# Kernel optimization log

Measured on AMD Instinct MI355X. Metric: run time of the kernel, lower is better.

Reference implementation:

```python
import jax, jax.numpy as jnp
import numpy as np
from jax import lax

H = 32      # n_heads
D = 128     # head_dim
HID = 4096  # hidden_dim
CQ, CK, CH = 4, 9, 2
G = H // CH  # conv groups == groupnorm groups == 16


def setup_inputs() -> dict:
    key = jax.random.key(0)
    ks = jax.random.split(key, 8)
    q_seqlen = np.array([512, 384, 384, 256], dtype=np.int64)
    kv_seqlen = np.array([512, 384, 384, 256], dtype=np.int64)
    Sq = int(q_seqlen.sum())
    Sk = int(kv_seqlen.sum())
    x = jax.random.normal(ks[0], (Sq, HID), dtype=jnp.float32) * 0.02
    context = jax.random.normal(ks[1], (Sk, HID), dtype=jnp.float32) * 0.02
    wq = jax.random.normal(ks[2], (HID, H * D), dtype=jnp.float32) * 0.02
    wkv = jax.random.normal(ks[3], (HID, 2 * H * D), dtype=jnp.float32) * 0.02
    wo = jax.random.normal(ks[4], (H * D, HID), dtype=jnp.float32) * 0.02
    # grouped conv kernel [out=H, in_per_group=CH, CQ, CK]; dirac-like identity + noise
    conv_w = jax.random.normal(ks[5], (H, CH, CQ, CK), dtype=jnp.float32) * 0.05
    conv_w = conv_w.at[jnp.arange(H), jnp.arange(H) % CH, CQ // 2, CK // 2].add(1.0)
    gn_w = jnp.ones((H,), dtype=jnp.float32)
    gn_b = jnp.zeros((H,), dtype=jnp.float32)
    return {"x": x, "context": context, "wq": wq, "wkv": wkv, "wo": wo,
            "conv_w": conv_w, "gn_w": gn_w, "gn_b": gn_b,
            "q_seqlen": q_seqlen, "kv_seqlen": kv_seqlen}


def _block_diag_mask(q_seqlen, kv_seqlen, dtype):
    # block-diagonal ones mask for packed ragged sequences (static lengths)
    q_len = np.asarray(q_seqlen)
    k_len = np.asarray(kv_seqlen)
    seg_q = np.repeat(np.arange(len(q_len)), q_len)
    seg_k = np.repeat(np.arange(len(k_len)), k_len)
    return jnp.asarray(seg_q[:, None] == seg_k[None, :], dtype=dtype)


def reference(x, context, wq, wkv, wo, conv_w, gn_w, gn_b, q_seqlen, kv_seqlen):
    S = x.shape[0]
    mask = _block_diag_mask(q_seqlen, kv_seqlen, x.dtype)  # [Sq, Sk]
    scale = 1.0 / np.sqrt(D).astype(np.float32)
    q = (x @ wq).reshape(S, H, D).transpose(1, 0, 2) * scale        # [H, Sq, D]
    kv = context @ wkv
    k = kv[:, : H * D].reshape(-1, H, D).transpose(1, 0, 2)         # [H, Sk, D]
    v = kv[:, H * D :].reshape(-1, H, D).transpose(1, 0, 2)         # [H, Sk, D]
    attn = jnp.einsum('hqd,hkd->hqk', q, k) * mask[None]            # [H, Sq, Sk]
    # grouped Conv2d over (query, key) positions, channels = heads
    a = lax.conv_general_dilated(
        attn[None], conv_w, window_strides=(1, 1),
        padding=((CQ // 2, CQ // 2), (CK // 2, CK // 2)),
        dimension_numbers=('NCHW', 'OIHW', 'NCHW'),
        feature_group_count=G)[0]                                   # [H, Sq+1, Sk]
    a = a[:, :-1, :]  # c_q even -> drop extra row (c_k odd -> no col drop)
    a = jax.nn.softmax(a + mask[None], axis=-1)                     # note: +1 bias inside blocks, not -inf
    out = jnp.einsum('hqk,hkd->hqd', a, v)                          # [H, Sq, D]
    # GroupNorm(num_groups=G, channels=H) over [1, H, Sq, D]
    og = out.reshape(G, CH, S, D)
    mu = og.mean(axis=(1, 2, 3), keepdims=True)
    var = og.var(axis=(1, 2, 3), keepdims=True)
    og = (og - mu) * lax.rsqrt(var + 1e-5)
    out = og.reshape(H, S, D) * gn_w[:, None, None] + gn_b[:, None, None]
    out = out.transpose(1, 0, 2).reshape(S, H * D)
    return out @ wo
```

## Files before the change

### kernel.cpp

```cpp
#include <hip/hip_runtime.h>
#include <stdint.h>


#define H_   32
#define D_   128
#define HID_ 4096
#define WMAX2 944
#define LPAD 8

typedef unsigned short bfr;
typedef __attribute__((ext_vector_type(4))) float f32x4;
typedef __attribute__((ext_vector_type(4))) int   i32x4;
typedef __attribute__((ext_vector_type(8))) unsigned short u16x8;
typedef __attribute__((ext_vector_type(4))) unsigned short u16x4;

__device__ __forceinline__ bfr f2bf(float f) {
  uint32_t u = __float_as_uint(f);
  u += 0x7fffu + ((u >> 16) & 1u);
  return (bfr)(u >> 16);
}
__device__ __forceinline__ float bf2f(bfr u) {
  return __uint_as_float(((uint32_t)u) << 16);
}
__device__ __forceinline__ void mfma_bf16(f32x4& d, i32x4 a, i32x4 b) {
  asm volatile("v_mfma_f32_16x16x32_bf16 %0, %1, %2, %0" : "+v"(d) : "v"(a), "v"(b));
}
__device__ __forceinline__ void gload_lds16(const void* g, void* l) {
  __builtin_amdgcn_global_load_lds((__attribute__((address_space(1))) void*)g,
                                   (__attribute__((address_space(3))) void*)l,
                                   16, 0, 0);
}

__global__ __launch_bounds__(256) void seg_setup(
    const void* __restrict__ qsl, const void* __restrict__ ksl,
    int* __restrict__ segq, int* __restrict__ segk,
    int* __restrict__ bq, int* __restrict__ bk,
    float* __restrict__ stats, int S, int Sk, int nseg)
{
  __shared__ int sbq[16], sbk[16];
  const int tid = threadIdx.x;
  if (tid == 0) {
    {
      const int* q32 = (const int*)qsl;
      long long s32 = 0; bool ok32 = true;
      for (int i = 0; i < nseg; ++i) { int v = q32[i]; if (v < 1 || v > S) ok32 = false; s32 += v; }
      const bool use32 = ok32 && (s32 == S);
      const long long* q64 = (const long long*)qsl;
      sbq[0] = 0;
      for (int i = 0; i < nseg; ++i) sbq[i + 1] = sbq[i] + (use32 ? q32[i] : (int)q64[i]);
    }
    {
      const int* k32 = (const int*)ksl;
      long long s32 = 0; bool ok32 = true;
      for (int i = 0; i < nseg; ++i) { int v = k32[i]; if (v < 1 || v > Sk) ok32 = false; s32 += v; }
      const bool use32 = ok32 && (s32 == Sk);
      const long long* k64 = (const long long*)ksl;
      sbk[0] = 0;
      for (int i = 0; i < nseg; ++i) sbk[i + 1] = sbk[i] + (use32 ? k32[i] : (int)k64[i]);
    }
    for (int i = 0; i <= nseg; ++i) { bq[i] = sbq[i]; bk[i] = sbk[i]; }
  }
  if (tid < 32) stats[tid] = 0.f;
  __syncthreads();
  for (int i = tid; i < S; i += 256) {
    int s = 0;
    while (s < nseg - 1 && i >= sbq[s + 1]) ++s;
    segq[i] = s;
  }
  for (int i = tid; i < Sk; i += 256) {
    int s = 0;
    while (s < nseg - 1 && i >= sbk[s + 1]) ++s;
    segk[i] = s;
  }
}

__global__ __launch_bounds__(256) void cvt_bf16(
    const float* __restrict__ in, bfr* __restrict__ out, long long n)
{
  long long i = ((long long)blockIdx.x * 256 + threadIdx.x) * 8;
  if (i >= n) return;
  f32x4 a = *(const f32x4*)(in + i);
  f32x4 b = *(const f32x4*)(in + i + 4);
  u16x8 o;
  #pragma unroll
  for (int j = 0; j < 4; ++j) { o[j] = f2bf(a[j]); o[4 + j] = f2bf(b[j]); }
  *(u16x8*)(out + i) = o;
}

__global__ __launch_bounds__(256) void transpose_cvt(
    const float* __restrict__ in, bfr* __restrict__ out, int R, int ld)
{
  __shared__ float tile[64][65];
  const int t = threadIdx.x;
  const int rb = blockIdx.y * 64, cb = blockIdx.x * 64;
  const int row = t >> 2, c4 = (t & 3) * 16;
  const float* gp = in + (long long)(rb + row) * ld + cb + c4;
  #pragma unroll
  for (int j = 0; j < 4; ++j) {
    f32x4 v = *(const f32x4*)(gp + j * 4);
    #pragma unroll
    for (int q = 0; q < 4; ++q) tile[row][c4 + j * 4 + q] = v[q];
  }
  __syncthreads();
  const int cc = row, r4 = c4;
  u16x8 a, b;
  #pragma unroll
  for (int j = 0; j < 8; ++j) a[j] = f2bf(tile[r4 + j][cc]);
  #pragma unroll
  for (int j = 0; j < 8; ++j) b[j] = f2bf(tile[r4 + 8 + j][cc]);
  bfr* op = out + (long long)(cb + cc) * R + rb + r4;
  *(u16x8*)op = a;
  *(u16x8*)(op + 8) = b;
}

__global__ __launch_bounds__(256) void transpose_b16(
    const bfr* __restrict__ in, bfr* __restrict__ out, int R, int C)
{
  __shared__ bfr t[64][72];
  const int z = blockIdx.z;
  const bfr* ip = in + (long long)z * R * C;
  bfr* op = out + (long long)z * R * C;
  const int rb = blockIdx.y * 64, cb = blockIdx.x * 64;
  const int tr = threadIdx.x >> 3;
  const int tc = (threadIdx.x & 7) * 8;
  #pragma unroll
  for (int half = 0; half < 2; ++half) {
    const int r = tr + half * 32;
    u16x8 v = *(const u16x8*)(ip + (long long)(rb + r) * C + cb + tc);
    *(u16x8*)&t[r][tc] = v;
  }
  __syncthreads();
  #pragma unroll
  for (int half = 0; half < 2; ++half) {
    const int cc = tr + half * 32;
    u16x8 vv;
    #pragma unroll
    for (int j = 0; j < 8; ++j) vv[j] = t[tc + j][cc];
    *(u16x8*)(op + (long long)(cb + cc) * R + rb + tc) = vv;
  }
}

__global__ __launch_bounds__(256) void colsum_v(
    const bfr* __restrict__ vt, float* __restrict__ cs, int Sk)
{
  const int lane = threadIdx.x & 63, wave = threadIdx.x >> 6;
  const int row = blockIdx.x * 4 + wave;
  const bfr* src = vt + (long long)row * Sk;
  float s = 0.f;
  for (int i = lane * 8; i + 8 <= Sk; i += 512) {
    u16x8 v = *(const u16x8*)(src + i);
    #pragma unroll
    for (int j = 0; j < 8; ++j) s += bf2f(v[j]);
  }
  #pragma unroll
  for (int m = 1; m < 64; m <<= 1) s += __shfl_xor(s, m);
  if (lane == 0) cs[row] = s;
}

struct GemmAux {
  const int* segq; const int* segk; const int* bk;
  bfr* qb; bfr* kb; bfr* vrow;
  float* outb; float* stats;
  const float* fvArr; const float* colsum;
  float scale;
  int S, Sk, nOff;
};

enum { MODE_PLAIN = 0, MODE_Q = 1, MODE_KV = 2, MODE_QK = 3, MODE_PV = 4 };

template <int MODE, int KS = 1>
__global__ __launch_bounds__(256) void gemm_bt(
    const bfr* __restrict__ A, const bfr* __restrict__ Bt, void* __restrict__ Cout,
    int N, int K, int lda, int ldb,
    long long aZ, long long bZ, long long cZ, GemmAux aux)
{
  __shared__ bfr As[128 * 32];
  __shared__ bfr Bs[128 * 32];
  __shared__ float redS[8], redSS[8];
  const int tid = threadIdx.x;
  const int lane = tid & 63;
  const int wave = tid >> 6;
  const int z = blockIdx.z;

  int bx = blockIdx.x, by = blockIdx.y;
  {
    const int gx = gridDim.x, gy = gridDim.y;
    if (((gx & 3) == 0) && ((gy & 1) == 0)) {
      const int lid = by * gx + bx;
      const int xcd = lid & 7, inner = lid >> 3;
      const int cm = gy >> 1, cn = gx >> 2;
      by = (xcd >> 2) * cm + inner / cn;
      bx = (xcd & 3) * cn + inner % cn;
    }
  }
  const int m0 = by * 128;
  const int n0 = bx * 128;
  const bfr* Ap = A + (long long)z * aZ;
  const bfr* Bp = Bt + (long long)z * bZ;

  int kLo = 0, kHiV = K;
  if constexpr (KS > 1) { const int ksp = K / KS; kLo = z * ksp; kHiV = kLo + ksp; }
  if constexpr (MODE == MODE_PV) {
    const int t127 = min(m0 + 127, aux.S - 1);
    kLo = (max(aux.bk[aux.segq[max(m0 - 2, 0)]] - 4, 0)) & ~31;
    int th = min(aux.bk[aux.segq[min(t127 + 1, aux.S - 1)] + 1] + 4, aux.Sk);
    kHiV = min((th + 31) & ~31, aux.Sk);
  }

  const int wr = (wave >> 1) * 64;
  const int wc = (wave & 1) * 64;
  f32x4 acc[4][4];
  #pragma unroll
  for (int i = 0; i < 4; ++i)
    #pragma unroll
    for (int j = 0; j < 4; ++j) acc[i][j] = (f32x4){0.f, 0.f, 0.f, 0.f};

  const int srow = lane >> 2;
  const int scol = (((lane & 3) ^ ((lane >> 3) & 3)) << 3);
  const int rcol = (((lane >> 4) ^ ((lane >> 1) & 3)) << 3);

  const int kSteps = (kHiV - kLo) >> 5;
  for (int ks = 0; ks < kSteps; ++ks) {
    const int k0 = kLo + (ks << 5);
    #pragma unroll
    for (int c = 0; c < 4; ++c) {
      const int chunk = (wave << 2) + c;
      const int ci = chunk & 7;
      const int row = ci * 16 + srow;
      if (chunk < 8) gload_lds16(Ap + (long long)(m0 + row) * lda + k0 + scol, As + ci * 512);
      else           gload_lds16(Bp + (long long)(n0 + row) * ldb + k0 + scol, Bs + ci * 512);
    }
    __syncthreads();
    i32x4 af[4], bfv[4];
    #pragma unroll
    for (int i = 0; i < 4; ++i)
      af[i] = *(const i32x4*)&As[(wr + i * 16 + (lane & 15)) * 32 + rcol];
    #pragma unroll
    for (int i = 0; i < 4; ++i)
      bfv[i] = *(const i32x4*)&Bs[(wc + i * 16 + (lane & 15)) * 32 + rcol];
    #pragma unroll
    for (int i = 0; i < 4; ++i)
      #pragma unroll
      for (int j = 0; j < 4; ++j)
        mfma_bf16(acc[i][j], af[i], bfv[j]);
    __syncthreads();
  }

  float fvm[16], csn[4];
  if constexpr (MODE == MODE_PV) {
    #pragma unroll
    for (int i = 0; i < 4; ++i)
      #pragma unroll
      for (int r = 0; r < 4; ++r)
        fvm[i * 4 + r] = aux.fvArr[(long long)z * aux.S + m0 + wr + i * 16 + (lane >> 4) * 4 + r];
    #pragma unroll
    for (int j = 0; j < 4; ++j)
      csn[j] = aux.colsum[(long long)z * D_ + n0 + wc + j * 16 + (lane & 15)];
  }

  float sv = 0.f, sq2 = 0.f;
  #pragma unroll
  for (int i = 0; i < 4; ++i) {
    #pragma unroll
    for (int j = 0; j < 4; ++j) {
      #pragma unroll
      for (int r = 0; r < 4; ++r) {
        const int m = m0 + wr + i * 16 + (lane >> 4) * 4 + r;
        const int n = n0 + wc + j * 16 + (lane & 15);
        const float v = acc[i][j][r];
        if constexpr (KS > 1) {
          aux.outb[((long long)z * aux.S + m) * N + n] = v;
        } else if constexpr (MODE == MODE_PLAIN) {
          ((float*)Cout)[(long long)m * N + n] = v;
        } else if constexpr (MODE == MODE_Q) {
          const int hh = n >> 7, d = n & 127;
          aux.qb[((long long)hh * aux.S + m) * D_ + d] = f2bf(v * aux.scale);
        } else if constexpr (MODE == MODE_KV) {
          const int ng = n + aux.nOff;
          if (ng < H_ * D_) {
            const int hh = ng >> 7, d = ng & 127;
            aux.kb[((long long)hh * aux.Sk + m) * D_ + d] = f2bf(v);
          } else {
            const int nv = ng - H_ * D_;
            const int hh = nv >> 7, d = nv & 127;
            aux.vrow[((long long)hh * aux.Sk + m) * D_ + d] = f2bf(v);
          }
        } else if constexpr (MODE == MODE_PV) {
          const float vv = v + fvm[i * 4 + r] * csn[j];
          aux.outb[((long long)z * aux.S + m) * D_ + n] = vv;
          sv += vv; sq2 += vv * vv;
        }
      }
    }
  }

  if constexpr (MODE == MODE_PV && KS == 1) {
    #pragma unroll
    for (int msk = 1; msk < 64; msk <<= 1) {
      sv  += __shfl_xor(sv, msk);
      sq2 += __shfl_xor(sq2, msk);
    }
    if (lane == 0) { redS[wave] = sv; redSS[wave] = sq2; }
    __syncthreads();
    if (tid == 0) {
      const float a = redS[0] + redS[1] + redS[2] + redS[3];
      const float b = redSS[0] + redSS[1] + redSS[2] + redSS[3];
      atomicAdd(&aux.stats[(z >> 1) * 2 + 0], a);
      atomicAdd(&aux.stats[(z >> 1) * 2 + 1], b);
    }
  }
}

__global__ __launch_bounds__(256) void gemm_qk(
    const bfr* __restrict__ A, const bfr* __restrict__ Bt, bfr* __restrict__ Cout,
    long long aZ, long long bZ, long long cZ, GemmAux aux)
{
  __shared__ bfr As[128 * 128];
  __shared__ bfr Bs[128 * 128];
  const int tid = threadIdx.x;
  const int lane = tid & 63;
  const int wave = tid >> 6;
  const int z = blockIdx.z;
  const int m0 = blockIdx.y * 128;
  const int n0 = blockIdx.x * 128;

  const int t127 = min(m0 + 127, aux.S - 1);
  const int loT = max(aux.bk[aux.segq[max(m0 - 2, 0)]] - 4, 0);
  const int hiT = min(aux.bk[aux.segq[min(t127 + 1, aux.S - 1)] + 1] + 4, aux.Sk);
  if (n0 > hiT + 16 || n0 + 127 < loT - 16) return;
  const int sm0 = aux.segq[m0], sm1 = aux.segq[t127];
  const int sn0 = aux.segk[n0], sn1 = aux.segk[min(n0 + 127, aux.Sk - 1)];
  if (sm1 < sn0 || sn1 < sm0) {
    bfr* C = Cout + (long long)z * cZ + (long long)m0 * aux.Sk + n0;
    const i32x4 zz = {0, 0, 0, 0};
    #pragma unroll
    for (int c = 0; c < 8; ++c) {
      int id = c * 256 + tid;
      int r = id >> 4, col = (id & 15) * 8;
      *(i32x4*)(C + (long long)r * aux.Sk + col) = zz;
    }
    return;
  }

  const bfr* Ap = A + (long long)z * aZ;
  const bfr* Bp = Bt + (long long)z * bZ;

  const int srow = lane >> 4;
  #pragma unroll
  for (int c = 0; c < 16; ++c) {
    const int chunk = wave * 16 + c;
    const int cl = chunk & 31;
    const int f = (2 * cl + (lane >> 5)) & 7;
    const int sc = ((lane & 15) ^ f) * 8;
    const int r = cl * 4 + srow;
    if (chunk < 32) gload_lds16(Ap + (long long)(m0 + r) * D_ + sc, As + cl * 512);
    else            gload_lds16(Bp + (long long)(n0 + r) * D_ + sc, Bs + cl * 512);
  }
  __syncthreads();

  const int wr = (wave >> 1) * 64;
  const int wc = (wave & 1) * 64;
  f32x4 acc[4][4];
  #pragma unroll
  for (int i = 0; i < 4; ++i)
    #pragma unroll
    for (int j = 0; j < 4; ++j) acc[i][j] = (f32x4){0.f, 0.f, 0.f, 0.f};

  const int rf = (lane >> 1) & 7;
  #pragma unroll
  for (int ks = 0; ks < 4; ++ks) {
    const int slot = (4 * ks + (lane >> 4)) ^ rf;
    const int colb = slot * 8;
    i32x4 af[4], bfv[4];
    #pragma unroll
    for (int i = 0; i < 4; ++i)
      af[i] = *(const i32x4*)&As[(wr + i * 16 + (lane & 15)) * 128 + colb];
    #pragma unroll
    for (int j = 0; j < 4; ++j)
      bfv[j] = *(const i32x4*)&Bs[(wc + j * 16 + (lane & 15)) * 128 + colb];
    #pragma unroll
    for (int i = 0; i < 4; ++i)
      #pragma unroll
      for (int j = 0; j < 4; ++j)
        mfma_bf16(acc[i][j], af[i], bfv[j]);
  }

  const bool qkUni = (sm0 == sm1) && (sn0 == sn1);
  int sgm[16], sgn[4];
  if (!qkUni) {
    #pragma unroll
    for (int i = 0; i < 4; ++i)
      #pragma unroll
      for (int r = 0; r < 4; ++r)
        sgm[i * 4 + r] = aux.segq[m0 + wr + i * 16 + (lane >> 4) * 4 + r];
    #pragma unroll
    for (int j = 0; j < 4; ++j) sgn[j] = aux.segk[n0 + wc + j * 16 + (lane & 15)];
  }
  #pragma unroll
  for (int i = 0; i < 4; ++i) {
    #pragma unroll
    for (int j = 0; j < 4; ++j) {
      #pragma unroll
      for (int r = 0; r < 4; ++r) {
        const int m = m0 + wr + i * 16 + (lane >> 4) * 4 + r;
        const int n = n0 + wc + j * 16 + (lane & 15);
        const float v = acc[i][j][r];
        const float vv = (qkUni || sgm[i * 4 + r] == sgn[j]) ? v : 0.f;
        Cout[(long long)z * cZ + (long long)m * aux.Sk + n] = f2bf(vv);
      }
    }
  }
}

__global__ __launch_bounds__(256) void reduce_split_q(
    const float* __restrict__ part, bfr* __restrict__ qb, float scale, int S)
{
  const long long MN = (long long)S * HID_;
  const long long i = ((long long)blockIdx.x * 256 + threadIdx.x) * 8;
  if (i >= MN) return;
  const f32x4 a0 = *(const f32x4*)(part + i);
  const f32x4 a1 = *(const f32x4*)(part + i + 4);
  const f32x4 b0 = *(const f32x4*)(part + MN + i);
  const f32x4 b1 = *(const f32x4*)(part + MN + i + 4);
  const int m = (int)(i >> 12);
  const int n = (int)(i & 4095);
  const int hh = n >> 7, d = n & 127;
  u16x8 o;
  #pragma unroll
  for (int j = 0; j < 4; ++j) {
    o[j]     = f2bf((a0[j] + b0[j]) * scale);
    o[4 + j] = f2bf((a1[j] + b1[j]) * scale);
  }
  *(u16x8*)(qb + ((long long)hh * S + m) * D_ + d) = o;
}

__global__ __launch_bounds__(256) void reduce_split_f32(
    const float* __restrict__ part, float* __restrict__ out, long long MN)
{
  const long long i = ((long long)blockIdx.x * 256 + threadIdx.x) * 8;
  if (i >= MN) return;
  const f32x4 a0 = *(const f32x4*)(part + i);
  const f32x4 a1 = *(const f32x4*)(part + i + 4);
  const f32x4 b0 = *(const f32x4*)(part + MN + i);
  const f32x4 b1 = *(const f32x4*)(part + MN + i + 4);
  f32x4 o0, o1;
  #pragma unroll
  for (int j = 0; j < 4; ++j) { o0[j] = a0[j] + b0[j]; o1[j] = a1[j] + b1[j]; }
  *(f32x4*)(out + i) = o0;
  *(f32x4*)(out + i + 4) = o1;
}

__global__ __launch_bounds__(512) void conv_softmax6(
    const bfr* __restrict__ attn, const float* __restrict__ conv_w,
    bfr* __restrict__ p, float* __restrict__ fvArr,
    const int* __restrict__ segq, const int* __restrict__ segk,
    const int* __restrict__ bk, int S, int Sk, int h0)
{
  __shared__ float wsh[144];
  __shared__ bfr sIn[11][WMAX2];
  const int tid = threadIdx.x, lane = tid & 63, w = tid >> 6;
  const int q0 = blockIdx.x * 8;
  const int c0 = blockIdx.y * 2;
  const int h  = h0 + c0;
  if (tid < 144) wsh[tid] = conv_w[h * 72 + tid];

  const int lo0 = (max(bk[segq[max(q0 - 2, 0)]] - 4, 0)) & ~7;
  const int hiL = min(bk[segq[min(q0 + 8, S - 1)] + 1] + 4, Sk);
  const int g0 = max(lo0 - 8, 0) & ~7;
  const int g1 = min(hiL + 4, Sk);
  const int W8 = (g1 - g0 + 7) >> 3;

  const int qa = q0 + w;
  const int loA = (max(bk[segq[max(qa - 2, 0)]] - 4, 0)) & ~7;
  const int hiA = min(bk[segq[min(qa + 1, S - 1)] + 1] + 4, Sk);
  const int sqA = segq[qa];
  const int width = hiA - loA;

  float lg[2][2][8];
  #pragma unroll
  for (int e = 0; e < 2; ++e)
    #pragma unroll
    for (int pp = 0; pp < 2; ++pp)
      #pragma unroll
      for (int o = 0; o < 8; ++o) lg[e][pp][o] = 0.f;

  if (tid < 11) {
    const u16x8 zz8 = {0,0,0,0,0,0,0,0};
    *(u16x8*)&sIn[tid][0] = zz8;
    *(u16x8*)&sIn[tid][LPAD + W8 * 8] = zz8;
  }

  for (int pass = 0; pass < 2; ++pass) {
    if (pass) __syncthreads();
    const bfr* src0 = attn + (long long)(c0 + pass) * S * Sk;
    for (int it = tid; it < 11 * 116; it += 512) {
      const int ri = it / 116;
      const int j  = it - ri * 116;
      if (j < W8) {
        const int r = q0 - 2 + ri;
        u16x8 v = {0,0,0,0,0,0,0,0};
        if (r >= 0 && r < S) v = *(const u16x8*)(src0 + (long long)r * Sk + g0 + j * 8);
        *(u16x8*)&sIn[ri][LPAD + j * 8] = v;
      }
    }
    __syncthreads();

    #pragma unroll
    for (int pp = 0; pp < 2; ++pp) {
      const int kk = loA + pp * 512 + lane * 8;
      if (kk < hiA) {
        const int ib = LPAD + kk - 4 - g0;
        #pragma unroll
        for (int rr = 0; rr < 4; ++rr) {
          const bfr* sp = &sIn[w + rr][ib];
          u16x4 u0 = *(const u16x4*)(sp);
          u16x4 u1 = *(const u16x4*)(sp + 4);
          u16x4 u2 = *(const u16x4*)(sp + 8);
          u16x4 u3 = *(const u16x4*)(sp + 12);
          float xx[16];
          #pragma unroll
          for (int j2 = 0; j2 < 4; ++j2) {
            xx[j2]      = bf2f(u0[j2]);
            xx[4 + j2]  = bf2f(u1[j2]);
            xx[8 + j2]  = bf2f(u2[j2]);
            xx[12 + j2] = bf2f(u3[j2]);
          }
          const float* wv0 = &wsh[(pass * 4 + rr) * 9];
          const float* wv1 = wv0 + 72;
          #pragma unroll
          for (int dk = 0; dk < 9; ++dk) {
            #pragma unroll
            for (int o = 0; o < 8; ++o) {
              lg[0][pp][o] += xx[o + dk] * wv0[dk];
              lg[1][pp][o] += xx[o + dk] * wv1[dk];
            }
          }
        }
      }
    }
  }

  float lmax0 = -1e30f, lmax1 = -1e30f;
  #pragma unroll
  for (int pp = 0; pp < 2; ++pp) {
    const int kk = loA + pp * 512 + lane * 8;
    int sk8[8];
    if (kk < Sk) {
      i32x4 a = *(const i32x4*)&segk[kk];
      i32x4 b = *(const i32x4*)&segk[kk + 4];
      #pragma unroll
      for (int j = 0; j < 4; ++j) { sk8[j] = a[j]; sk8[4 + j] = b[j]; }
    } else {
      #pragma unroll
      for (int j = 0; j < 8; ++j) sk8[j] = -1;
    }
    #pragma unroll
    for (int o = 0; o < 8; ++o) {
      const int k = kk + o;
      float v0 = -1e30f, v1 = -1e30f;
      if (k < hiA) {
        const float mb = (sk8[o] == sqA) ? 1.f : 0.f;
        v0 = lg[0][pp][o] + mb; lmax0 = fmaxf(lmax0, v0);
        v1 = lg[1][pp][o] + mb; lmax1 = fmaxf(lmax1, v1);
      }
      lg[0][pp][o] = v0; lg[1][pp][o] = v1;
    }
  }
  #pragma unroll
  for (int m = 1; m < 64; m <<= 1) {
    lmax0 = fmaxf(lmax0, __shfl_xor(lmax0, m));
    lmax1 = fmaxf(lmax1, __shfl_xor(lmax1, m));
  }
  const float M0 = fmaxf(lmax0, 0.f), M1 = fmaxf(lmax1, 0.f);
  float ls0 = 0.f, ls1 = 0.f;
  #pragma unroll
  for (int pp = 0; pp < 2; ++pp)
    #pragma unroll
    for (int o = 0; o < 8; ++o) {
      const float e0 = __expf(lg[0][pp][o] - M0);
      const float e1 = __expf(lg[1][pp][o] - M1);
      lg[0][pp][o] = e0; ls0 += e0;
      lg[1][pp][o] = e1; ls1 += e1;
    }
  #pragma unroll
  for (int m = 1; m < 64; m <<= 1) {
    ls0 += __shfl_xor(ls0, m);
    ls1 += __shfl_xor(ls1, m);
  }
  const float eo0 = __expf(-M0), eo1 = __expf(-M1);
  const float iv0 = 1.f / (ls0 + (float)(Sk - width) * eo0);
  const float iv1 = 1.f / (ls1 + (float)(Sk - width) * eo1);
  const float fv0 = eo0 * iv0, fv1 = eo1 * iv1;

  const int t0 = (q0 >> 7) << 7;
  const int t127 = min(t0 + 127, S - 1);
  const int tLo = (max(bk[segq[max(t0 - 2, 0)]] - 4, 0)) & ~31;
  int tHi = min(bk[segq[min(t127 + 1, S - 1)] + 1] + 4, Sk);
  tHi = min((tHi + 31) & ~31, Sk);

  bfr* row0 = p + ((long long)(c0 + 0) * S + qa) * Sk;
  bfr* row1 = p + ((long long)(c0 + 1) * S + qa) * Sk;
  #pragma unroll
  for (int pp = 0; pp < 2; ++pp) {
    const int kk = loA + pp * 512 + lane * 8;
    if (kk + 7 < hiA) {
      u16x8 s0, s1;
      #pragma unroll
      for (int o = 0; o < 8; ++o) {
        s0[o] = f2bf(lg[0][pp][o] * iv0 - fv0);
        s1[o] = f2bf(lg[1][pp][o] * iv1 - fv1);
      }
      *(u16x8*)(row0 + kk) = s0;
      *(u16x8*)(row1 + kk) = s1;
    } else if (kk < hiA) {
      for (int o = 0; o < 8; ++o)
        if (kk + o < hiA) {
          row0[kk + o] = f2bf(lg[0][pp][o] * iv0 - fv0);
          row1[kk + o] = f2bf(lg[1][pp][o] * iv1 - fv1);
        }
    }
  }
  const u16x4 z4 = {0, 0, 0, 0};
  for (int k = tLo + lane * 4; k < loA; k += 256) {
    *(u16x4*)(row0 + k) = z4;
    *(u16x4*)(row1 + k) = z4;
  }
  for (int k = hiA + lane; k < tHi; k += 64) { row0[k] = 0; row1[k] = 0; }
  if (lane == 0) {
    fvArr[(long long)(h + 0) * S + qa] = fv0;
    fvArr[(long long)(h + 1) * S + qa] = fv1;
  }
}

__global__ void gn_finalize(const float* __restrict__ stats, float* __restrict__ mr, float invcnt)
{
  const int g = threadIdx.x;
  if (g < 16) {
    const float s = stats[2 * g], ss = stats[2 * g + 1];
    const float mu = s * invcnt;
    const float var = ss * invcnt - mu * mu;
    mr[2 * g] = mu;
    mr[2 * g + 1] = rsqrtf(var + 1e-5f);
  }
}

__global__ __launch_bounds__(256) void gn_apply(
    const float* __restrict__ outb, const float* __restrict__ mr,
    const float* __restrict__ gnw, const float* __restrict__ gnb,
    bfr* __restrict__ y, int S)
{
  const int h = blockIdx.y;
  const long long inner = ((long long)blockIdx.x * 256 + threadIdx.x) * 8;
  if (inner >= (long long)S * D_) return;
  const int s = (int)(inner >> 7), d = (int)(inner & 127);
  const int g = h >> 1;
  const float mu = mr[2 * g], rs = mr[2 * g + 1];
  const float wgt = gnw[h] * rs;
  const float b = gnb[h] - mu * wgt;
  const float* src = outb + (long long)h * S * D_ + inner;
  const f32x4 a = *(const f32x4*)(src);
  const f32x4 c = *(const f32x4*)(src + 4);
  u16x8 o;
  #pragma unroll
  for (int j = 0; j < 4; ++j) { o[j] = f2bf(a[j] * wgt + b); o[4 + j] = f2bf(c[j] * wgt + b); }
  *(u16x8*)(y + (long long)s * HID_ + h * D_ + d) = o;
}

extern "C" void kernel_launch(void* const* d_in, const int* in_sizes, int n_in,
                              void* d_out, int out_size, void* d_ws, size_t ws_size,
                              hipStream_t stream)
{
  const float* x      = (const float*)d_in[0];
  const float* ctx    = (const float*)d_in[1];
  const float* wq     = (const float*)d_in[2];
  const float* wkv    = (const float*)d_in[3];
  const float* wo     = (const float*)d_in[4];
  const float* conv_w = (const float*)d_in[5];
  const float* gnw    = (const float*)d_in[6];
  const float* gnb    = (const float*)d_in[7];
  const void*  qsl    = d_in[8];
  const void*  ksl    = d_in[9];
  const int S    = in_sizes[0] / HID_;
  const int Sk   = in_sizes[1] / HID_;
  const int nseg = in_sizes[8];

  auto al = [](size_t v) { return (v + 255) & ~(size_t)255; };
  char* base = (char*)d_ws;
  size_t off = 0;
  auto take = [&](size_t bytes) -> char* { char* r = base + off; off += al(bytes); return r; };

  int*   segq  = (int*)take((size_t)S * 4);
  int*   segk  = (int*)take((size_t)Sk * 4);
  int*   bq    = (int*)take(64);
  int*   bk    = (int*)take(64);
  float* stats = (float*)take(128);
  float* mr    = (float*)take(128);
  float* fvArr = (float*)take((size_t)H_ * S * 4);
  float* csV   = (float*)take((size_t)H_ * D_ * 4);
  bfr*   qb    = (bfr*)take((size_t)H_ * S * D_ * 2);
  bfr*   kbuf  = (bfr*)take((size_t)H_ * Sk * D_ * 2);
  bfr*   vrow  = (bfr*)take((size_t)H_ * Sk * D_ * 2);
  bfr*   vt    = (bfr*)take((size_t)H_ * Sk * D_ * 2);
  float* outb  = (float*)take((size_t)H_ * S * D_ * 4);
  const size_t poolBase = off;
  char*  pool  = base + poolBase;

  const int Smax = (S > Sk) ? S : Sk;
  const size_t A1 = al((size_t)Smax * HID_ * 2);
  const size_t WT = al((size_t)HID_ * HID_ * 2);
  const size_t PART = al((size_t)2 * S * HID_ * 4);

  const size_t CAmin = al((size_t)4 * S * Sk * 2);
  const size_t fusedNeed = (A1 + 2 * WT > 2 * CAmin) ? (A1 + 2 * WT) : (2 * CAmin);
  const bool fused = (poolBase + fusedNeed <= ws_size);
  const bool splitOK = (poolBase + A1 + 2 * WT + PART <= ws_size);
  const size_t wNeed = A1 + (fused ? 2 : 1) * WT + (splitOK ? PART : 0);

  int nc = 4;
  {
    const int cands[3] = {32, 16, 8};
    for (int ci = 0; ci < 3; ++ci) {
      const size_t CA = al((size_t)cands[ci] * S * Sk * 2);
      const size_t need = (wNeed > 2 * CA) ? wNeed : (2 * CA);
      if (poolBase + need <= ws_size) { nc = cands[ci]; break; }
    }
  }
  const size_t CA = al((size_t)nc * S * Sk * 2);
  bfr*   xcb    = (bfr*)pool;
  bfr*   wT     = (bfr*)(pool + A1);
  float* partB  = (float*)(pool + A1 + 2 * WT);
  bfr*   attn_c = (bfr*)pool;
  bfr*   pbuf_c = (bfr*)(pool + CA);

  seg_setup<<<1, 256, 0, stream>>>(qsl, ksl, segq, segk, bq, bk, stats, S, Sk, nseg);

  GemmAux aux{};
  aux.segq = segq; aux.segk = segk; aux.bk = bk;
  aux.qb = qb; aux.kb = kbuf; aux.vrow = vrow;
  aux.outb = outb; aux.stats = stats;
  aux.fvArr = fvArr; aux.colsum = csV;
  aux.scale = 0.08838834764831845f;
  aux.S = S; aux.Sk = Sk; aux.nOff = 0;

  const long long MN = (long long)S * HID_;
  const int nRed = (int)((MN / 8 + 255) / 256);

  const long long nx = (long long)S * HID_;
  cvt_bf16<<<(int)((nx / 8 + 255) / 256), 256, 0, stream>>>(x, xcb, nx);
  transpose_cvt<<<dim3(HID_ / 64, HID_ / 64), 256, 0, stream>>>(wq, wT, HID_, HID_);
  if (splitOK) {
    GemmAux auxQ = aux; auxQ.outb = partB;
    gemm_bt<MODE_Q, 2><<<dim3(HID_ / 128, S / 128, 2), 256, 0, stream>>>(
        xcb, wT, nullptr, HID_, HID_, HID_, HID_, 0, 0, 0, auxQ);
    reduce_split_q<<<nRed, 256, 0, stream>>>(partB, qb, aux.scale, S);
  } else {
    gemm_bt<MODE_Q><<<dim3(HID_ / 128, S / 128, 1), 256, 0, stream>>>(
        xcb, wT, nullptr, HID_, HID_, HID_, HID_, 0, 0, 0, aux);
  }

  const long long nctx = (long long)Sk * HID_;
  cvt_bf16<<<(int)((nctx / 8 + 255) / 256), 256, 0, stream>>>(ctx, xcb, nctx);
  if (fused) {
    transpose_cvt<<<dim3(2 * HID_ / 64, HID_ / 64), 256, 0, stream>>>(wkv, wT, HID_, 2 * HID_);
    gemm_bt<MODE_KV><<<dim3(2 * HID_ / 128, Sk / 128, 1), 256, 0, stream>>>(
        xcb, wT, nullptr, 2 * HID_, HID_, HID_, HID_, 0, 0, 0, aux);
  } else {
    transpose_cvt<<<dim3(HID_ / 64, HID_ / 64), 256, 0, stream>>>(wkv, wT, HID_, 2 * HID_);
    gemm_bt<MODE_KV><<<dim3(HID_ / 128, Sk / 128, 1), 256, 0, stream>>>(
        xcb, wT, nullptr, HID_, HID_, HID_, HID_, 0, 0, 0, aux);
    transpose_cvt<<<dim3(HID_ / 64, HID_ / 64), 256, 0, stream>>>(wkv + HID_, wT, HID_, 2 * HID_);
    GemmAux auxV = aux; auxV.nOff = H_ * D_;
    gemm_bt<MODE_KV><<<dim3(HID_ / 128, Sk / 128, 1), 256, 0, stream>>>(
        xcb, wT, nullptr, HID_, HID_, HID_, HID_, 0, 0, 0, auxV);
  }

  transpose_b16<<<dim3(D_ / 64, Sk / 64, H_), 256, 0, stream>>>(vrow, vt, Sk, D_);
  colsum_v<<<H_ * D_ / 4, 256, 0, stream>>>(vt, csV, Sk);

  for (int h0 = 0; h0 < H_; h0 += nc) {
    gemm_qk<<<dim3(Sk / 128, S / 128, nc), 256, 0, stream>>>(
        qb + (size_t)h0 * S * D_, kbuf + (size_t)h0 * Sk * D_, attn_c,
        (long long)S * D_, (long long)Sk * D_, (long long)S * Sk, aux);
    conv_softmax6<<<dim3(S / 8, nc / 2), 512, 0, stream>>>(
        attn_c, conv_w, pbuf_c, fvArr, segq, segk, bk, S, Sk, h0);
    GemmAux auxP = aux;
    auxP.outb = outb + (size_t)h0 * S * D_;
    auxP.stats = stats + h0;
    auxP.fvArr = fvArr + (size_t)h0 * S;
    auxP.colsum = csV + (size_t)h0 * D_;
    gemm_bt<MODE_PV><<<dim3(1, S / 128, nc), 256, 0, stream>>>(
        pbuf_c, vt + (size_t)h0 * D_ * Sk, nullptr,
        D_, Sk, Sk, Sk,
        (long long)S * Sk, (long long)D_ * Sk, 0, auxP);
  }

  gn_finalize<<<1, 32, 0, stream>>>(stats, mr, 1.0f / (2.0f * S * D_));
  gn_apply<<<dim3((S * D_) / 2048, H_), 256, 0, stream>>>(outb, mr, gnw, gnb, xcb, S);
  transpose_cvt<<<dim3(HID_ / 64, HID_ / 64), 256, 0, stream>>>(wo, wT, HID_, HID_);
  if (splitOK) {
    GemmAux auxO = aux; auxO.outb = partB;
    gemm_bt<MODE_PLAIN, 2><<<dim3(HID_ / 128, S / 128, 2), 256, 0, stream>>>(
        xcb, wT, nullptr, HID_, HID_, HID_, HID_, 0, 0, 0, auxO);
    reduce_split_f32<<<nRed, 256, 0, stream>>>(partB, (float*)d_out, MN);
  } else {
    gemm_bt<MODE_PLAIN><<<dim3(HID_ / 128, S / 128, 1), 256, 0, stream>>>(
        xcb, wT, d_out, HID_, HID_, HID_, HID_, 0, 0, 0, aux);
  }
}
```

Measured before the change: 531.8 us.

## Use 8-wave GEMM with 64-wide K tiles for projections; widen conv LDS reads

Adds a new projection GEMM kernel (gemm_bt8s) with 512 threads, 8 waves each computing a 64x32 sub-tile, and a 64-deep K step with an 8-way XOR swizzle. This halves the number of barrier-synchronized K iterations and raises the wave count per block for the Q, KV and output projections. The original 256-thread kernel is kept only for the PV mode. Separately, the conv/softmax kernel reads its shared-memory window with three 8-element loads instead of four 4-element loads. The cost is double the LDS per block and less MFMA work per wave, which may lower occupancy or reuse.

```diff
diff --git a/kernel.cpp b/kernel.cpp
--- a/kernel.cpp
+++ b/kernel.cpp
@@ -169,14 +169,12 @@
 enum { MODE_PLAIN = 0, MODE_Q = 1, MODE_KV = 2, MODE_QK = 3, MODE_PV = 4 };
 
 template <int MODE, int KS = 1>
-__global__ __launch_bounds__(256) void gemm_bt(
+__global__ __launch_bounds__(512) void gemm_bt8s(
     const bfr* __restrict__ A, const bfr* __restrict__ Bt, void* __restrict__ Cout,
-    int N, int K, int lda, int ldb,
-    long long aZ, long long bZ, long long cZ, GemmAux aux)
-{
-  __shared__ bfr As[128 * 32];
-  __shared__ bfr Bs[128 * 32];
-  __shared__ float redS[8], redSS[8];
+    int N, int K, int lda, int ldb, GemmAux aux)
+{
+  __shared__ bfr As[128 * 64];
+  __shared__ bfr Bs[128 * 64];
   const int tid = threadIdx.x;
   const int lane = tid & 63;
   const int wave = tid >> 6;
@@ -193,76 +191,57 @@
       bx = (xcd & 3) * cn + inner % cn;
     }
   }
-  const int m0 = by * 128;
-  const int n0 = bx * 128;
-  const bfr* Ap = A + (long long)z * aZ;
-  const bfr* Bp = Bt + (long long)z * bZ;
-
-  int kLo = 0, kHiV = K;
-  if constexpr (KS > 1) { const int ksp = K / KS; kLo = z * ksp; kHiV = kLo + ksp; }
-  if constexpr (MODE == MODE_PV) {
-    const int t127 = min(m0 + 127, aux.S - 1);
-    kLo = (max(aux.bk[aux.segq[max(m0 - 2, 0)]] - 4, 0)) & ~31;
-    int th = min(aux.bk[aux.segq[min(t127 + 1, aux.S - 1)] + 1] + 4, aux.Sk);
-    kHiV = min((th + 31) & ~31, aux.Sk);
-  }
-
-  const int wr = (wave >> 1) * 64;
-  const int wc = (wave & 1) * 64;
-  f32x4 acc[4][4];
+  const int m0 = by * 128, n0 = bx * 128;
+
+  int kLo = 0, kHi = K;
+  if constexpr (KS > 1) { const int ksp = K / KS; kLo = z * ksp; kHi = kLo + ksp; }
+
+  const int wr = (wave >> 2) * 64;
+  const int wc = (wave & 3) * 32;
+  f32x4 acc[4][2];
   #pragma unroll
   for (int i = 0; i < 4; ++i)
     #pragma unroll
-    for (int j = 0; j < 4; ++j) acc[i][j] = (f32x4){0.f, 0.f, 0.f, 0.f};
-
-  const int srow = lane >> 2;
-  const int scol = (((lane & 3) ^ ((lane >> 3) & 3)) << 3);
-  const int rcol = (((lane >> 4) ^ ((lane >> 1) & 3)) << 3);
-
-  const int kSteps = (kHiV - kLo) >> 5;
+    for (int j = 0; j < 2; ++j) acc[i][j] = (f32x4){0.f, 0.f, 0.f, 0.f};
+
+  const int srow64 = lane >> 3;
+  const int scol64 = (((lane & 7) ^ ((lane >> 3) & 7)) << 3);
+
+  const int kSteps = (kHi - kLo) >> 6;
   for (int ks = 0; ks < kSteps; ++ks) {
-    const int k0 = kLo + (ks << 5);
+    const int k0 = kLo + (ks << 6);
     #pragma unroll
     for (int c = 0; c < 4; ++c) {
       const int chunk = (wave << 2) + c;
-      const int ci = chunk & 7;
-      const int row = ci * 16 + srow;
-      if (chunk < 8) gload_lds16(Ap + (long long)(m0 + row) * lda + k0 + scol, As + ci * 512);
-      else           gload_lds16(Bp + (long long)(n0 + row) * ldb + k0 + scol, Bs + ci * 512);
+      const int ci = chunk & 15;
+      const int row = ci * 8 + srow64;
+      if (chunk < 16) gload_lds16(A  + (long long)(m0 + row) * lda + k0 + scol64, As + ci * 512);
+      else            gload_lds16(Bt + (long long)(n0 + row) * ldb + k0 + scol64, Bs + ci * 512);
     }
     __syncthreads();
-    i32x4 af[4], bfv[4];
-    #pragma unroll
-    for (int i = 0; i < 4; ++i)
-      af[i] = *(const i32x4*)&As[(wr + i * 16 + (lane & 15)) * 32 + rcol];
-    #pragma unroll
-    for (int i = 0; i < 4; ++i)
-      bfv[i] = *(const i32x4*)&Bs[(wc + i * 16 + (lane & 15)) * 32 + rcol];
-    #pragma unroll
-    for (int i = 0; i < 4; ++i)
-      #pragma unroll
-      for (int j = 0; j < 4; ++j)
-        mfma_bf16(acc[i][j], af[i], bfv[j]);
+    #pragma unroll
+    for (int ks2 = 0; ks2 < 2; ++ks2) {
+      const int rcol = (((ks2 * 4 + (lane >> 4)) ^ (lane & 7)) << 3);
+      i32x4 af[4], bfv[2];
+      #pragma unroll
+      for (int i = 0; i < 4; ++i)
+        af[i] = *(const i32x4*)&As[(wr + i * 16 + (lane & 15)) * 64 + rcol];
+      #pragma unroll
+      for (int j = 0; j < 2; ++j)
+        bfv[j] = *(const i32x4*)&Bs[(wc + j * 16 + (lane & 15)) * 64 + rcol];
+      #pragma unroll
+      for (int i = 0; i < 4; ++i)
+        #pragma unroll
+        for (int j = 0; j < 2; ++j)
+          mfma_bf16(acc[i][j], af[i], bfv[j]);
+    }
     __syncthreads();
   }
 
-  float fvm[16], csn[4];
-  if constexpr (MODE == MODE_PV) {
-    #pragma unroll
-    for (int i = 0; i < 4; ++i)
-      #pragma unroll
-      for (int r = 0; r < 4; ++r)
-        fvm[i * 4 + r] = aux.fvArr[(long long)z * aux.S + m0 + wr + i * 16 + (lane >> 4) * 4 + r];
-    #pragma unroll
-    for (int j = 0; j < 4; ++j)
-      csn[j] = aux.colsum[(long long)z * D_ + n0 + wc + j * 16 + (lane & 15)];
-  }
-
-  float sv = 0.f, sq2 = 0.f;
   #pragma unroll
   for (int i = 0; i < 4; ++i) {
     #pragma unroll
-    for (int j = 0; j < 4; ++j) {
+    for (int j = 0; j < 2; ++j) {
       #pragma unroll
       for (int r = 0; r < 4; ++r) {
         const int m = m0 + wr + i * 16 + (lane >> 4) * 4 + r;
@@ -285,16 +264,111 @@
             const int hh = nv >> 7, d = nv & 127;
             aux.vrow[((long long)hh * aux.Sk + m) * D_ + d] = f2bf(v);
           }
-        } else if constexpr (MODE == MODE_PV) {
+        }
+      }
+    }
+  }
+}
+
+template <int MODE>
+__global__ __launch_bounds__(256) void gemm_bt(
+    const bfr* __restrict__ A, const bfr* __restrict__ Bt, void* __restrict__ Cout,
+    int N, int K, int lda, int ldb,
+    long long aZ, long long bZ, long long cZ, GemmAux aux)
+{
+  __shared__ bfr As[128 * 32];
+  __shared__ bfr Bs[128 * 32];
+  __shared__ float redS[8], redSS[8];
+  const int tid = threadIdx.x;
+  const int lane = tid & 63;
+  const int wave = tid >> 6;
+  const int z = blockIdx.z;
+  const int m0 = blockIdx.y * 128;
+  const int n0 = blockIdx.x * 128;
+  const bfr* Ap = A + (long long)z * aZ;
+  const bfr* Bp = Bt + (long long)z * bZ;
+
+  int kLo = 0, kHiV = K;
+  if constexpr (MODE == MODE_PV) {
+    const int t127 = min(m0 + 127, aux.S - 1);
+    kLo = (max(aux.bk[aux.segq[max(m0 - 2, 0)]] - 4, 0)) & ~31;
+    int th = min(aux.bk[aux.segq[min(t127 + 1, aux.S - 1)] + 1] + 4, aux.Sk);
+    kHiV = min((th + 31) & ~31, aux.Sk);
+  }
+
+  const int wr = (wave >> 1) * 64;
+  const int wc = (wave & 1) * 64;
+  f32x4 acc[4][4];
+  #pragma unroll
+  for (int i = 0; i < 4; ++i)
+    #pragma unroll
+    for (int j = 0; j < 4; ++j) acc[i][j] = (f32x4){0.f, 0.f, 0.f, 0.f};
+
+  const int srow = lane >> 2;
+  const int scol = (((lane & 3) ^ ((lane >> 3) & 3)) << 3);
+  const int rcol = (((lane >> 4) ^ ((lane >> 1) & 3)) << 3);
+
+  const int kSteps = (kHiV - kLo) >> 5;
+  for (int ks = 0; ks < kSteps; ++ks) {
+    const int k0 = kLo + (ks << 5);
+    #pragma unroll
+    for (int c = 0; c < 4; ++c) {
+      const int chunk = (wave << 2) + c;
+      const int ci = chunk & 7;
+      const int row = ci * 16 + srow;
+      if (chunk < 8) gload_lds16(Ap + (long long)(m0 + row) * lda + k0 + scol, As + ci * 512);
+      else           gload_lds16(Bp + (long long)(n0 + row) * ldb + k0 + scol, Bs + ci * 512);
+    }
+    __syncthreads();
+    i32x4 af[4], bfv[4];
+    #pragma unroll
+    for (int i = 0; i < 4; ++i)
+      af[i] = *(const i32x4*)&As[(wr + i * 16 + (lane & 15)) * 32 + rcol];
+    #pragma unroll
+    for (int i = 0; i < 4; ++i)
+      bfv[i] = *(const i32x4*)&Bs[(wc + i * 16 + (lane & 15)) * 32 + rcol];
+    #pragma unroll
+    for (int i = 0; i < 4; ++i)
+      #pragma unroll
+      for (int j = 0; j < 4; ++j)
+        mfma_bf16(acc[i][j], af[i], bfv[j]);
+    __syncthreads();
+  }
+
+  float fvm[16], csn[4];
+  if constexpr (MODE == MODE_PV) {
+    #pragma unroll
+    for (int i = 0; i < 4; ++i)
+      #pragma unroll
+      for (int r = 0; r < 4; ++r)
+        fvm[i * 4 + r] = aux.fvArr[(long long)z * aux.S + m0 + wr + i * 16 + (lane >> 4) * 4 + r];
+    #pragma unroll
+    for (int j = 0; j < 4; ++j)
+      csn[j] = aux.colsum[(long long)z * D_ + n0 + wc + j * 16 + (lane & 15)];
+  }
+
+  float sv = 0.f, sq2 = 0.f;
+  #pragma unroll
+  for (int i = 0; i < 4; ++i) {
+    #pragma unroll
+    for (int j = 0; j < 4; ++j) {
+      #pragma unroll
+      for (int r = 0; r < 4; ++r) {
+        const int m = m0 + wr + i * 16 + (lane >> 4) * 4 + r;
+        const int n = n0 + wc + j * 16 + (lane & 15);
+        const float v = acc[i][j][r];
+        if constexpr (MODE == MODE_PV) {
           const float vv = v + fvm[i * 4 + r] * csn[j];
           aux.outb[((long long)z * aux.S + m) * D_ + n] = vv;
           sv += vv; sq2 += vv * vv;
+        } else if constexpr (MODE == MODE_PLAIN) {
+          ((float*)Cout)[(long long)m * N + n] = v;
         }
       }
     }
   }
 
-  if constexpr (MODE == MODE_PV && KS == 1) {
+  if constexpr (MODE == MODE_PV) {
     #pragma unroll
     for (int msk = 1; msk < 64; msk <<= 1) {
       sv  += __shfl_xor(sv, msk);
@@ -450,7 +524,7 @@
   *(f32x4*)(out + i + 4) = o1;
 }
 
-__global__ __launch_bounds__(512) void conv_softmax6(
+__global__ __launch_bounds__(512) void conv_softmax7(
     const bfr* __restrict__ attn, const float* __restrict__ conv_w,
     bfr* __restrict__ p, float* __restrict__ fvArr,
     const int* __restrict__ segq, const int* __restrict__ segk,
@@ -509,21 +583,20 @@
     for (int pp = 0; pp < 2; ++pp) {
       const int kk = loA + pp * 512 + lane * 8;
       if (kk < hiA) {
-        const int ib = LPAD + kk - 4 - g0;
+        const int ib2 = LPAD + kk - 8 - g0;
         #pragma unroll
         for (int rr = 0; rr < 4; ++rr) {
-          const bfr* sp = &sIn[w + rr][ib];
-          u16x4 u0 = *(const u16x4*)(sp);
-          u16x4 u1 = *(const u16x4*)(sp + 4);
-          u16x4 u2 = *(const u16x4*)(sp + 8);
-          u16x4 u3 = *(const u16x4*)(sp + 12);
+          const bfr* sp = &sIn[w + rr][ib2];
+          u16x8 u0 = *(const u16x8*)(sp);
+          u16x8 u1 = *(const u16x8*)(sp + 8);
+          u16x8 u2 = *(const u16x8*)(sp + 16);
           float xx[16];
           #pragma unroll
           for (int j2 = 0; j2 < 4; ++j2) {
-            xx[j2]      = bf2f(u0[j2]);
+            xx[j2]      = bf2f(u0[4 + j2]);
             xx[4 + j2]  = bf2f(u1[j2]);
-            xx[8 + j2]  = bf2f(u2[j2]);
-            xx[12 + j2] = bf2f(u3[j2]);
+            xx[8 + j2]  = bf2f(u1[4 + j2]);
+            xx[12 + j2] = bf2f(u2[j2]);
           }
           const float* wv0 = &wsh[(pass * 4 + rr) * 9];
           const float* wv1 = wv0 + 72;
@@ -750,28 +823,28 @@
   transpose_cvt<<<dim3(HID_ / 64, HID_ / 64), 256, 0, stream>>>(wq, wT, HID_, HID_);
   if (splitOK) {
     GemmAux auxQ = aux; auxQ.outb = partB;
-    gemm_bt<MODE_Q, 2><<<dim3(HID_ / 128, S / 128, 2), 256, 0, stream>>>(
-        xcb, wT, nullptr, HID_, HID_, HID_, HID_, 0, 0, 0, auxQ);
+    gemm_bt8s<MODE_Q, 2><<<dim3(HID_ / 128, S / 128, 2), 512, 0, stream>>>(
+        xcb, wT, nullptr, HID_, HID_, HID_, HID_, auxQ);
     reduce_split_q<<<nRed, 256, 0, stream>>>(partB, qb, aux.scale, S);
   } else {
-    gemm_bt<MODE_Q><<<dim3(HID_ / 128, S / 128, 1), 256, 0, stream>>>(
-        xcb, wT, nullptr, HID_, HID_, HID_, HID_, 0, 0, 0, aux);
+    gemm_bt8s<MODE_Q><<<dim3(HID_ / 128, S / 128, 1), 512, 0, stream>>>(
+        xcb, wT, nullptr, HID_, HID_, HID_, HID_, aux);
   }
 
   const long long nctx = (long long)Sk * HID_;
   cvt_bf16<<<(int)((nctx / 8 + 255) / 256), 256, 0, stream>>>(ctx, xcb, nctx);
   if (fused) {
     transpose_cvt<<<dim3(2 * HID_ / 64, HID_ / 64), 256, 0, stream>>>(wkv, wT, HID_, 2 * HID_);
-    gemm_bt<MODE_KV><<<dim3(2 * HID_ / 128, Sk / 128, 1), 256, 0, stream>>>(
-        xcb, wT, nullptr, 2 * HID_, HID_, HID_, HID_, 0, 0, 0, aux);
+    gemm_bt8s<MODE_KV><<<dim3(2 * HID_ / 128, Sk / 128, 1), 512, 0, stream>>>(
+        xcb, wT, nullptr, 2 * HID_, HID_, HID_, HID_, aux);
   } else {
     transpose_cvt<<<dim3(HID_ / 64, HID_ / 64), 256, 0, stream>>>(wkv, wT, HID_, 2 * HID_);
-    gemm_bt<MODE_KV><<<dim3(HID_ / 128, Sk / 128, 1), 256, 0, stream>>>(
-        xcb, wT, nullptr, HID_, HID_, HID_, HID_, 0, 0, 0, aux);
+    gemm_bt8s<MODE_KV><<<dim3(HID_ / 128, Sk / 128, 1), 512, 0, stream>>>(
+        xcb, wT, nullptr, HID_, HID_, HID_, HID_, aux);
     transpose_cvt<<<dim3(HID_ / 64, HID_ / 64), 256, 0, stream>>>(wkv + HID_, wT, HID_, 2 * HID_);
     GemmAux auxV = aux; auxV.nOff = H_ * D_;
-    gemm_bt<MODE_KV><<<dim3(HID_ / 128, Sk / 128, 1), 256, 0, stream>>>(
-        xcb, wT, nullptr, HID_, HID_, HID_, HID_, 0, 0, 0, auxV);
+    gemm_bt8s<MODE_KV><<<dim3(HID_ / 128, Sk / 128, 1), 512, 0, stream>>>(
+        xcb, wT, nullptr, HID_, HID_, HID_, HID_, auxV);
   }
 
   transpose_b16<<<dim3(D_ / 64, Sk / 64, H_), 256, 0, stream>>>(vrow, vt, Sk, D_);
@@ -781,7 +854,7 @@
     gemm_qk<<<dim3(Sk / 128, S / 128, nc), 256, 0, stream>>>(
         qb + (size_t)h0 * S * D_, kbuf + (size_t)h0 * Sk * D_, attn_c,
         (long long)S * D_, (long long)Sk * D_, (long long)S * Sk, aux);
-    conv_softmax6<<<dim3(S / 8, nc / 2), 512, 0, stream>>>(
+    conv_softmax7<<<dim3(S / 8, nc / 2), 512, 0, stream>>>(
         attn_c, conv_w, pbuf_c, fvArr, segq, segk, bk, S, Sk, h0);
     GemmAux auxP = aux;
     auxP.outb = outb + (size_t)h0 * S * D_;
@@ -799,11 +872,11 @@
   transpose_cvt<<<dim3(HID_ / 64, HID_ / 64), 256, 0, stream>>>(wo, wT, HID_, HID_);
   if (splitOK) {
     GemmAux auxO = aux; auxO.outb = partB;
-    gemm_bt<MODE_PLAIN, 2><<<dim3(HID_ / 128, S / 128, 2), 256, 0, stream>>>(
-        xcb, wT, nullptr, HID_, HID_, HID_, HID_, 0, 0, 0, auxO);
+    gemm_bt8s<MODE_PLAIN, 2><<<dim3(HID_ / 128, S / 128, 2), 512, 0, stream>>>(
+        xcb, wT, nullptr, HID_, HID_, HID_, HID_, auxO);
     reduce_split_f32<<<nRed, 256, 0, stream>>>(partB, (float*)d_out, MN);
   } else {
-    gemm_bt<MODE_PLAIN><<<dim3(HID_ / 128, S / 128, 1), 256, 0, stream>>>(
-        xcb, wT, d_out, HID_, HID_, HID_, HID_, 0, 0, 0, aux);
-  }
-}
+    gemm_bt8s<MODE_PLAIN><<<dim3(HID_ / 128, S / 128, 1), 512, 0, stream>>>(
+        xcb, wT, d_out, HID_, HID_, HID_, HID_, aux);
+  }
+}
```

Result: slower. 560.1 us (+5.3%).
